# Kernel optimization log

Measured on AMD Instinct MI355X. Metric: run time of the kernel, lower is better.

## Reference

```python
import jax, jax.numpy as jnp
import numpy as np

TEMPERATURE = 0.5
LOSS_WEIGHT = 0.2
EPS = 1e-8


def setup_inputs() -> dict:
    key = jax.random.key(0)
    k1, k2 = jax.random.split(key)
    L, B, H = 4, 256, 65536
    hidden_states = jax.random.normal(k1, (L, B, H), dtype=jnp.float32)
    task_type = jax.random.randint(k2, (B,), 0, 16, dtype=jnp.int64)
    return {"hidden_states": hidden_states, "task_type": task_type}


def reference(hidden_states, task_type):
    # hidden_states: [L, B, H] stacked flattened intermediate activations
    # (world_size == 1, so the gathered global states equal the local states)
    L, B, H = hidden_states.shape
    # F.normalize(p=2, dim=2)
    x = hidden_states / jnp.maximum(
        jnp.linalg.norm(hidden_states, axis=2, keepdims=True), 1e-12)

    # pos_mask from task-type equality, diagonal (self-pairs) zeroed
    pos_mask = (task_type[:, None] == task_type[None, :]).astype(x.dtype)
    pos_mask = pos_mask * (1.0 - jnp.eye(B, dtype=x.dtype))  # [B, B]

    # cdist(..., compute_mode='use_mm_for_euclid_dist') ** 2:
    # ||xi||^2 + ||xj||^2 - 2 xi.xj, clamped at 0
    sq = jnp.sum(x * x, axis=2)                      # [L, B]
    dots = jnp.einsum('lbh,lch->lbc', x, x)          # [L, B, B] -- dominant GEMM
    d2 = jnp.maximum(sq[:, :, None] + sq[:, None, :] - 2.0 * dots, 0.0)

    w = jnp.exp(-(d2 / TEMPERATURE))                 # [L, B, B]
    a = jnp.sum(w * pos_mask[None], axis=2)          # [L, B]
    b = jnp.sum(w, axis=2)                           # [L, B]
    per_layer = -jnp.mean(jnp.log((a + EPS) / (b + EPS)), axis=1)  # [L]
    return jnp.sum(per_layer) / L * LOSS_WEIGHT
```

## Files before the change

kernel.cpp:

```cpp
#include <hip/hip_runtime.h>
#include <hip/hip_bf16.h>

#define L_LAYERS 4
#define B_DIM 256
#define H_DIM 65536
#define KC 1024
#define BK 64
#define NKT (KC / BK)
#define NKZ (H_DIM / KC)
#define NSLICE (L_LAYERS * NKZ)
#define LDSTR 72

using bf16x8_t = __attribute__((ext_vector_type(8))) short;
using shortx8  = __attribute__((ext_vector_type(8))) short;
using shortx4  = __attribute__((ext_vector_type(4))) short;
using floatx4  = __attribute__((ext_vector_type(4))) float;

__device__ __forceinline__ unsigned short f2bf(float f) {
    unsigned u = __float_as_uint(f);
    return (unsigned short)((u + 0x7fffu + ((u >> 16) & 1u)) >> 16);
}

__global__ __launch_bounds__(512, 2) void gram_kernel(const float* __restrict__ hs,
                                                      short* __restrict__ S) {
    __shared__ short lds[B_DIM * LDSTR];

    const int tid = threadIdx.x;
    const int bx  = blockIdx.x;
    const int l   = bx >> 6;
    const int kz  = bx & (NKZ - 1);

    const int wave = tid >> 6, lane = tid & 63;
    const int wm = wave >> 1;
    const int wn = wave & 1;
    const int mrow = lane & 15, quad = lane >> 4;

    const int r = tid >> 1;
    const int h = tid & 1;
    const float* gp = hs + ((size_t)l * B_DIM + r) * H_DIM + (size_t)kz * KC + h * 32;
    const int ldsw = r * LDSTR + h * 32;

    floatx4 acc[4][8];
#pragma unroll
    for (int i = 0; i < 4; ++i)
#pragma unroll
        for (int j = 0; j < 8; ++j) acc[i][j] = (floatx4)0.0f;

    float4 pv[8];
#pragma unroll
    for (int q = 0; q < 8; ++q) pv[q] = *(const float4*)(gp + q * 4);

    for (int kt = 0; kt < NKT; ++kt) {
#pragma unroll
        for (int q = 0; q < 4; ++q) {
            shortx8 w;
            w[0] = (short)f2bf(pv[2 * q].x);     w[1] = (short)f2bf(pv[2 * q].y);
            w[2] = (short)f2bf(pv[2 * q].z);     w[3] = (short)f2bf(pv[2 * q].w);
            w[4] = (short)f2bf(pv[2 * q + 1].x); w[5] = (short)f2bf(pv[2 * q + 1].y);
            w[6] = (short)f2bf(pv[2 * q + 1].z); w[7] = (short)f2bf(pv[2 * q + 1].w);
            *(shortx8*)&lds[ldsw + q * 8] = w;
        }

        if (kt < NKT - 1) {
            const float* gn = gp + (kt + 1) * BK;
#pragma unroll
            for (int q = 0; q < 8; ++q) pv[q] = *(const float4*)(gn + q * 4);
        }
        __syncthreads();

#pragma unroll
        for (int kk = 0; kk < 2; ++kk) {
            bf16x8_t af[4], bfv[8];
#pragma unroll
            for (int i = 0; i < 4; ++i)
                af[i] = *(const bf16x8_t*)&lds[(wm * 64 + i * 16 + mrow) * LDSTR + kk * 32 + quad * 8];
#pragma unroll
            for (int j = 0; j < 8; ++j)
                bfv[j] = *(const bf16x8_t*)&lds[(wn * 128 + j * 16 + mrow) * LDSTR + kk * 32 + quad * 8];
#pragma unroll
            for (int i = 0; i < 4; ++i)
#pragma unroll
                for (int j = 0; j < 8; ++j)
                    acc[i][j] = __builtin_amdgcn_mfma_f32_16x16x32_bf16(af[i], bfv[j], acc[i][j], 0, 0, 0);
        }
        __syncthreads();
    }

    short* Ssl = S + (size_t)bx * (B_DIM * B_DIM);
#pragma unroll
    for (int i = 0; i < 4; ++i) {
        const int row0 = wm * 64 + i * 16 + quad * 4;
#pragma unroll
        for (int j = 0; j < 8; ++j) {
            const int col = wn * 128 + j * 16 + mrow;
            shortx4 v;
            v[0] = (short)f2bf(acc[i][j][0]);
            v[1] = (short)f2bf(acc[i][j][1]);
            v[2] = (short)f2bf(acc[i][j][2]);
            v[3] = (short)f2bf(acc[i][j][3]);
            *(shortx4*)&Ssl[(size_t)col * B_DIM + row0] = v;
        }
    }
}

__global__ __launch_bounds__(128) void reduce_kernel(const short* __restrict__ S,
                                                     float* __restrict__ G) {
    const int li = blockIdx.x;
    const int j2 = threadIdx.x;
    const int l  = li >> 8;
    const int i  = li & 255;
    const unsigned* base = (const unsigned*)(S + ((size_t)l * NKZ) * (B_DIM * B_DIM) + i * B_DIM) + j2;
    float s0 = 0.0f, s1 = 0.0f;
#pragma unroll
    for (int kz = 0; kz < NKZ; ++kz) {
        const unsigned u = base[(size_t)kz * (B_DIM * B_DIM / 2)];
        s0 += __uint_as_float(u << 16);
        s1 += __uint_as_float(u & 0xffff0000u);
    }
    float2 out;
    out.x = s0;
    out.y = s1;
    *(float2*)(G + (size_t)li * B_DIM + 2 * j2) = out;
}

__global__ __launch_bounds__(256) void loss_kernel(const float* __restrict__ G,
                                                   const int* __restrict__ task,
                                                   float* __restrict__ out) {
    const int i = blockIdx.x, l = blockIdx.y, j = threadIdx.x;

    __shared__ int s_odd_nz;
    if (j == 0) s_odd_nz = 0;
    __syncthreads();
    if (j < 128 && task[2 * j + 1] != 0) s_odd_nz = 1;
    __syncthreads();
    const bool is64 = (s_odd_nz == 0);

    const float* Gl = G + (size_t)l * B_DIM * B_DIM;
    const float gij = Gl[i * B_DIM + j];
    const float gii = Gl[i * B_DIM + i];
    const float gjj = Gl[j * B_DIM + j];
    const float nd  = gij * rsqrtf(gii) * rsqrtf(gjj);
    const float d2  = fmaxf(2.0f - 2.0f * nd, 0.0f);
    const float w   = __expf(-2.0f * d2);

    const int ti = is64 ? task[2 * i] : task[i];
    const int tj = is64 ? task[2 * j] : task[j];
    const float pm = (ti == tj && i != j) ? 1.0f : 0.0f;

    float a = w * pm, b = w;
#pragma unroll
    for (int off = 32; off > 0; off >>= 1) {
        a += __shfl_down(a, off);
        b += __shfl_down(b, off);
    }
    __shared__ float sa[4], sb[4];
    const int wv = j >> 6, ln = j & 63;
    if (ln == 0) { sa[wv] = a; sb[wv] = b; }
    __syncthreads();
    if (j == 0) {
        const float A  = sa[0] + sa[1] + sa[2] + sa[3];
        const float Bb = sb[0] + sb[1] + sb[2] + sb[3];
        const float c  = -logf((A + 1e-8f) / (Bb + 1e-8f)) * (0.2f / 1024.0f);
        atomicAdd(out, c);
    }
}

extern "C" void kernel_launch(void* const* d_in, const int* in_sizes, int n_in,
                              void* d_out, int out_size, void* d_ws, size_t ws_size,
                              hipStream_t stream) {
    const float* hs   = (const float*)d_in[0];
    const int*   task = (const int*)d_in[1];
    float*       out  = (float*)d_out;

    short* S = (short*)d_ws;
    float* G = (float*)(S + (size_t)NSLICE * (B_DIM * B_DIM));

    hipMemsetAsync(out, 0, sizeof(float), stream);

    gram_kernel<<<dim3(NSLICE), dim3(512), 0, stream>>>(hs, S);
    reduce_kernel<<<dim3(L_LAYERS * B_DIM), dim3(128), 0, stream>>>(S, G);
    loss_kernel<<<dim3(B_DIM, L_LAYERS), dim3(256), 0, stream>>>(G, task, out);
}
```

Measured before the change: 415.5 us.

## Fuse gram, split-K reduction and loss into one cooperative kernel

Merges the three kernels into a single cooperative launch of 256 blocks, using grid-wide syncs between the GEMM, the split-K reduction and the loss stage. The reduction keeps each block's rows in LDS and writes only the diagonal to global memory, so the full float Gram matrix is never materialised. This removes two kernel launches and the G round trip, but adds grid barrier overhead and requires all 256 blocks to be co-resident.

```diff
diff --git a/kernel.cpp b/kernel.cpp
--- a/kernel.cpp
+++ b/kernel.cpp
@@ -1,5 +1,8 @@
 #include <hip/hip_runtime.h>
 #include <hip/hip_bf16.h>
+#include <hip/hip_cooperative_groups.h>
+
+namespace cg = cooperative_groups;
 
 #define L_LAYERS 4
 #define B_DIM 256
@@ -21,147 +24,176 @@
     return (unsigned short)((u + 0x7fffu + ((u >> 16) & 1u)) >> 16);
 }
 
-__global__ __launch_bounds__(512, 2) void gram_kernel(const float* __restrict__ hs,
-                                                      short* __restrict__ S) {
+__global__ __launch_bounds__(512, 2) void fused_kernel(const float* __restrict__ hs,
+                                                       const int* __restrict__ task,
+                                                       float* __restrict__ out,
+                                                       short* __restrict__ S,
+                                                       float* __restrict__ diag) {
     __shared__ short lds[B_DIM * LDSTR];
+    __shared__ float sa[8], sb[8];
+    __shared__ int s_odd_nz;
+
+    cg::grid_group grid = cg::this_grid();
 
     const int tid = threadIdx.x;
     const int bx  = blockIdx.x;
     const int l   = bx >> 6;
     const int kz  = bx & (NKZ - 1);
 
-    const int wave = tid >> 6, lane = tid & 63;
-    const int wm = wave >> 1;
-    const int wn = wave & 1;
-    const int mrow = lane & 15, quad = lane >> 4;
-
-    const int r = tid >> 1;
-    const int h = tid & 1;
-    const float* gp = hs + ((size_t)l * B_DIM + r) * H_DIM + (size_t)kz * KC + h * 32;
-    const int ldsw = r * LDSTR + h * 32;
-
-    floatx4 acc[4][8];
-#pragma unroll
-    for (int i = 0; i < 4; ++i)
-#pragma unroll
-        for (int j = 0; j < 8; ++j) acc[i][j] = (floatx4)0.0f;
-
-    float4 pv[8];
-#pragma unroll
-    for (int q = 0; q < 8; ++q) pv[q] = *(const float4*)(gp + q * 4);
-
-    for (int kt = 0; kt < NKT; ++kt) {
-#pragma unroll
+    {
+        const int wave = tid >> 6, lane = tid & 63;
+        const int wm = wave >> 1;
+        const int wn = wave & 1;
+        const int mrow = lane & 15, quad = lane >> 4;
+
+        const int r = tid >> 1;
+        const int h = tid & 1;
+        const float* gp = hs + ((size_t)l * B_DIM + r) * H_DIM + (size_t)kz * KC + h * 32;
+        const int ldsw = r * LDSTR + h * 32;
+
+        floatx4 acc[4][8];
+#pragma unroll
+        for (int i = 0; i < 4; ++i)
+#pragma unroll
+            for (int j = 0; j < 8; ++j) acc[i][j] = (floatx4)0.0f;
+
+        float4 pv[8];
+#pragma unroll
+        for (int q = 0; q < 8; ++q) pv[q] = *(const float4*)(gp + q * 4);
+
+        for (int kt = 0; kt < NKT; ++kt) {
+#pragma unroll
+            for (int q = 0; q < 4; ++q) {
+                shortx8 w;
+                w[0] = (short)f2bf(pv[2 * q].x);     w[1] = (short)f2bf(pv[2 * q].y);
+                w[2] = (short)f2bf(pv[2 * q].z);     w[3] = (short)f2bf(pv[2 * q].w);
+                w[4] = (short)f2bf(pv[2 * q + 1].x); w[5] = (short)f2bf(pv[2 * q + 1].y);
+                w[6] = (short)f2bf(pv[2 * q + 1].z); w[7] = (short)f2bf(pv[2 * q + 1].w);
+                *(shortx8*)&lds[ldsw + q * 8] = w;
+            }
+            if (kt < NKT - 1) {
+                const float* gn = gp + (kt + 1) * BK;
+#pragma unroll
+                for (int q = 0; q < 8; ++q) pv[q] = *(const float4*)(gn + q * 4);
+            }
+            __syncthreads();
+
+#pragma unroll
+            for (int kk = 0; kk < 2; ++kk) {
+                bf16x8_t af[4], bfv[8];
+#pragma unroll
+                for (int i = 0; i < 4; ++i)
+                    af[i] = *(const bf16x8_t*)&lds[(wm * 64 + i * 16 + mrow) * LDSTR + kk * 32 + quad * 8];
+#pragma unroll
+                for (int j = 0; j < 8; ++j)
+                    bfv[j] = *(const bf16x8_t*)&lds[(wn * 128 + j * 16 + mrow) * LDSTR + kk * 32 + quad * 8];
+#pragma unroll
+                for (int i = 0; i < 4; ++i)
+#pragma unroll
+                    for (int j = 0; j < 8; ++j)
+                        acc[i][j] = __builtin_amdgcn_mfma_f32_16x16x32_bf16(af[i], bfv[j], acc[i][j], 0, 0, 0);
+            }
+            __syncthreads();
+        }
+
+        short* Ssl = S + (size_t)bx * (B_DIM * B_DIM);
+#pragma unroll
+        for (int i = 0; i < 4; ++i) {
+            const int row0 = wm * 64 + i * 16 + quad * 4;
+#pragma unroll
+            for (int j = 0; j < 8; ++j) {
+                const int col = wn * 128 + j * 16 + mrow;
+                shortx4 v;
+                v[0] = (short)f2bf(acc[i][j][0]);
+                v[1] = (short)f2bf(acc[i][j][1]);
+                v[2] = (short)f2bf(acc[i][j][2]);
+                v[3] = (short)f2bf(acc[i][j][3]);
+                *(shortx4*)&Ssl[(size_t)col * B_DIM + row0] = v;
+            }
+        }
+    }
+
+    __threadfence();
+    grid.sync();
+
+    float*  rowsL = (float*)lds;
+    float2* red   = (float2*)(lds + 2048);
+
+    const int z  = tid >> 7;
+    const int j2 = tid & 127;
+    {
+#pragma unroll 1
         for (int q = 0; q < 4; ++q) {
-            shortx8 w;
-            w[0] = (short)f2bf(pv[2 * q].x);     w[1] = (short)f2bf(pv[2 * q].y);
-            w[2] = (short)f2bf(pv[2 * q].z);     w[3] = (short)f2bf(pv[2 * q].w);
-            w[4] = (short)f2bf(pv[2 * q + 1].x); w[5] = (short)f2bf(pv[2 * q + 1].y);
-            w[6] = (short)f2bf(pv[2 * q + 1].z); w[7] = (short)f2bf(pv[2 * q + 1].w);
-            *(shortx8*)&lds[ldsw + q * 8] = w;
-        }
-
-        if (kt < NKT - 1) {
-            const float* gn = gp + (kt + 1) * BK;
-#pragma unroll
-            for (int q = 0; q < 8; ++q) pv[q] = *(const float4*)(gn + q * 4);
-        }
-        __syncthreads();
-
-#pragma unroll
-        for (int kk = 0; kk < 2; ++kk) {
-            bf16x8_t af[4], bfv[8];
-#pragma unroll
-            for (int i = 0; i < 4; ++i)
-                af[i] = *(const bf16x8_t*)&lds[(wm * 64 + i * 16 + mrow) * LDSTR + kk * 32 + quad * 8];
-#pragma unroll
-            for (int j = 0; j < 8; ++j)
-                bfv[j] = *(const bf16x8_t*)&lds[(wn * 128 + j * 16 + mrow) * LDSTR + kk * 32 + quad * 8];
-#pragma unroll
-            for (int i = 0; i < 4; ++i)
-#pragma unroll
-                for (int j = 0; j < 8; ++j)
-                    acc[i][j] = __builtin_amdgcn_mfma_f32_16x16x32_bf16(af[i], bfv[j], acc[i][j], 0, 0, 0);
-        }
-        __syncthreads();
+            const int job = bx * 4 + q;
+            const int jl  = job >> 8;
+            const int ji  = job & 255;
+            const unsigned* bp = (const unsigned*)S
+                + (size_t)(jl * NKZ + z * 16) * (B_DIM * B_DIM / 2)
+                + ji * (B_DIM / 2) + j2;
+            float s0 = 0.0f, s1 = 0.0f;
+#pragma unroll
+            for (int t = 0; t < 16; ++t) {
+                const unsigned u = bp[(size_t)t * (B_DIM * B_DIM / 2)];
+                s0 += __uint_as_float(u << 16);
+                s1 += __uint_as_float(u & 0xffff0000u);
+            }
+            red[z * 128 + j2] = float2{s0, s1};
+            __syncthreads();
+            if (z == 0) {
+                const float2 p0 = red[j2], p1 = red[128 + j2], p2 = red[256 + j2], p3 = red[384 + j2];
+                const float g0 = p0.x + p1.x + p2.x + p3.x;
+                const float g1 = p0.y + p1.y + p2.y + p3.y;
+                rowsL[q * 256 + 2 * j2]     = g0;
+                rowsL[q * 256 + 2 * j2 + 1] = g1;
+                if (2 * j2 == ji)     diag[jl * 256 + ji] = g0;
+                if (2 * j2 + 1 == ji) diag[jl * 256 + ji] = g1;
+            }
+            __syncthreads();
+        }
     }
 
-    short* Ssl = S + (size_t)bx * (B_DIM * B_DIM);
-#pragma unroll
-    for (int i = 0; i < 4; ++i) {
-        const int row0 = wm * 64 + i * 16 + quad * 4;
-#pragma unroll
-        for (int j = 0; j < 8; ++j) {
-            const int col = wn * 128 + j * 16 + mrow;
-            shortx4 v;
-            v[0] = (short)f2bf(acc[i][j][0]);
-            v[1] = (short)f2bf(acc[i][j][1]);
-            v[2] = (short)f2bf(acc[i][j][2]);
-            v[3] = (short)f2bf(acc[i][j][3]);
-            *(shortx4*)&Ssl[(size_t)col * B_DIM + row0] = v;
-        }
-    }
-}
-
-__global__ __launch_bounds__(128) void reduce_kernel(const short* __restrict__ S,
-                                                     float* __restrict__ G) {
-    const int li = blockIdx.x;
-    const int j2 = threadIdx.x;
-    const int l  = li >> 8;
-    const int i  = li & 255;
-    const unsigned* base = (const unsigned*)(S + ((size_t)l * NKZ) * (B_DIM * B_DIM) + i * B_DIM) + j2;
-    float s0 = 0.0f, s1 = 0.0f;
-#pragma unroll
-    for (int kz = 0; kz < NKZ; ++kz) {
-        const unsigned u = base[(size_t)kz * (B_DIM * B_DIM / 2)];
-        s0 += __uint_as_float(u << 16);
-        s1 += __uint_as_float(u & 0xffff0000u);
-    }
-    float2 out;
-    out.x = s0;
-    out.y = s1;
-    *(float2*)(G + (size_t)li * B_DIM + 2 * j2) = out;
-}
-
-__global__ __launch_bounds__(256) void loss_kernel(const float* __restrict__ G,
-                                                   const int* __restrict__ task,
-                                                   float* __restrict__ out) {
-    const int i = blockIdx.x, l = blockIdx.y, j = threadIdx.x;
-
-    __shared__ int s_odd_nz;
-    if (j == 0) s_odd_nz = 0;
+    __threadfence();
+    grid.sync();
+
+    if (tid == 0) s_odd_nz = 0;
     __syncthreads();
-    if (j < 128 && task[2 * j + 1] != 0) s_odd_nz = 1;
+    if (tid < 128 && task[2 * tid + 1] != 0) s_odd_nz = 1;
     __syncthreads();
     const bool is64 = (s_odd_nz == 0);
 
-    const float* Gl = G + (size_t)l * B_DIM * B_DIM;
-    const float gij = Gl[i * B_DIM + j];
-    const float gii = Gl[i * B_DIM + i];
-    const float gjj = Gl[j * B_DIM + j];
-    const float nd  = gij * rsqrtf(gii) * rsqrtf(gjj);
-    const float d2  = fmaxf(2.0f - 2.0f * nd, 0.0f);
-    const float w   = __expf(-2.0f * d2);
-
-    const int ti = is64 ? task[2 * i] : task[i];
-    const int tj = is64 ? task[2 * j] : task[j];
-    const float pm = (ti == tj && i != j) ? 1.0f : 0.0f;
-
-    float a = w * pm, b = w;
-#pragma unroll
-    for (int off = 32; off > 0; off >>= 1) {
-        a += __shfl_down(a, off);
-        b += __shfl_down(b, off);
-    }
-    __shared__ float sa[4], sb[4];
-    const int wv = j >> 6, ln = j & 63;
-    if (ln == 0) { sa[wv] = a; sb[wv] = b; }
-    __syncthreads();
-    if (j == 0) {
-        const float A  = sa[0] + sa[1] + sa[2] + sa[3];
-        const float Bb = sb[0] + sb[1] + sb[2] + sb[3];
-        const float c  = -logf((A + 1e-8f) / (Bb + 1e-8f)) * (0.2f / 1024.0f);
-        atomicAdd(out, c);
+#pragma unroll 1
+    for (int q = 0; q < 4; ++q) {
+        const int job = bx * 4 + q;
+        const int jl  = job >> 8;
+        const int ji  = job & 255;
+        float a = 0.0f, b = 0.0f;
+        if (tid < 256) {
+            const int j   = tid;
+            const float gij = rowsL[q * 256 + j];
+            const float gii = diag[jl * 256 + ji];
+            const float gjj = diag[jl * 256 + j];
+            const float nd  = gij * rsqrtf(gii) * rsqrtf(gjj);
+            const float d2  = fmaxf(2.0f - 2.0f * nd, 0.0f);
+            const float w   = __expf(-2.0f * d2);
+            const int ti = is64 ? task[2 * ji] : task[ji];
+            const int tj = is64 ? task[2 * j]  : task[j];
+            const float pm = (ti == tj && ji != j) ? 1.0f : 0.0f;
+            a = w * pm; b = w;
+        }
+#pragma unroll
+        for (int off = 32; off > 0; off >>= 1) {
+            a += __shfl_down(a, off);
+            b += __shfl_down(b, off);
+        }
+        const int wv = tid >> 6, ln = tid & 63;
+        if (ln == 0) { sa[wv] = a; sb[wv] = b; }
+        __syncthreads();
+        if (tid == 0) {
+            const float A  = sa[0] + sa[1] + sa[2] + sa[3] + sa[4] + sa[5] + sa[6] + sa[7];
+            const float Bb = sb[0] + sb[1] + sb[2] + sb[3] + sb[4] + sb[5] + sb[6] + sb[7];
+            atomicAdd(out, -logf((A + 1e-8f) / (Bb + 1e-8f)) * (0.2f / 1024.0f));
+        }
+        __syncthreads();
     }
 }
 
@@ -172,12 +204,11 @@
     const int*   task = (const int*)d_in[1];
     float*       out  = (float*)d_out;
 
-    short* S = (short*)d_ws;
-    float* G = (float*)(S + (size_t)NSLICE * (B_DIM * B_DIM));
+    short* S    = (short*)d_ws;
+    float* diag = (float*)(S + (size_t)NSLICE * (B_DIM * B_DIM));
 
     hipMemsetAsync(out, 0, sizeof(float), stream);
 
-    gram_kernel<<<dim3(NSLICE), dim3(512), 0, stream>>>(hs, S);
-    reduce_kernel<<<dim3(L_LAYERS * B_DIM), dim3(128), 0, stream>>>(S, G);
-    loss_kernel<<<dim3(B_DIM, L_LAYERS), dim3(256), 0, stream>>>(G, task, out);
+    void* args[] = { (void*)&hs, (void*)&task, (void*)&out, (void*)&S, (void*)&diag };
+    hipLaunchCooperativeKernel(fused_kernel, dim3(NSLICE), dim3(512), args, 0, stream);
 }
```

Result: slower. 599.9 us (+44.4%).
